# Optimization experiments

Measured on AMD Instinct MI355X. Metric: run time of the kernel, lower is better.

The kernel has to match this reference:

```python
import jax, jax.numpy as jnp
import numpy as np

N = 100000   # nodes
M = N - 1    # tree edges (child -> parent)
EMB = 512    # embedding_size
ENC = 512    # encoder_size


def setup_inputs() -> dict:
    key = jax.random.key(0)
    ks = jax.random.split(key, 10)
    x = jax.random.normal(ks[0], (N, EMB), jnp.float32)
    h = jax.random.normal(ks[1], (N, ENC), jnp.float32)
    c = jax.random.normal(ks[2], (N, ENC), jnp.float32)
    child_idx = jax.random.randint(ks[3], (M,), 0, N)
    parent_idx = jax.random.randint(ks[4], (M,), 0, N)
    s = 0.05
    W_iou = jax.random.normal(ks[5], (3 * ENC, EMB), jnp.float32) * s
    U_iou = jax.random.normal(ks[6], (3 * ENC, ENC), jnp.float32) * s
    b_iou = jnp.zeros((3 * ENC,), jnp.float32)
    U_f_w = jax.random.normal(ks[7], (ENC, ENC), jnp.float32) * s
    U_f_b = jax.random.normal(ks[8], (ENC,), jnp.float32) * s
    return {"x": x, "h": h, "c": c, "child_idx": child_idx,
            "parent_idx": parent_idx, "W_iou": W_iou, "U_iou": U_iou,
            "b_iou": b_iou, "U_f_w": U_f_w, "U_f_b": U_f_b}


def reference(x, h, c, child_idx, parent_idx, W_iou, U_iou, b_iou, U_f_w, U_f_b):
    n = x.shape[0]
    # message_func: gather child states along edges  [M, ENC]
    h_src = h[child_idx]
    c_src = c[child_idx]
    # reduce_func: forget gate per child, ragged sums over children
    f = jax.nn.sigmoid(h_src @ U_f_w.T + U_f_b)               # [M, ENC]
    h_tilde = jax.ops.segment_sum(h_src, parent_idx, num_segments=n)
    c_red = jax.ops.segment_sum(f * c_src, parent_idx, num_segments=n)
    deg = jax.ops.segment_sum(jnp.ones((h_src.shape[0],), x.dtype),
                              parent_idx, num_segments=n)
    has_child = (deg > 0)[:, None]
    # reduce_func overwrites iou with U_iou(h_tilde) for nodes with children;
    # leaves keep the initial W_iou(x).
    iou = jnp.where(has_child, h_tilde @ U_iou.T, x @ W_iou.T) + b_iou
    i, o, u = jnp.split(iou, 3, axis=1)
    c_new = jax.nn.sigmoid(i) * jnp.tanh(u) + jnp.where(has_child, c_red, 0.0)
    h_new = jax.nn.sigmoid(o) * jnp.tanh(c_new)
    return h_new, c_new
```

## Files before the change

kernel.cpp:

```cpp
#include <hip/hip_runtime.h>
#include <stdint.h>

typedef __bf16 bf16x8 __attribute__((ext_vector_type(8)));
typedef float f32x4 __attribute__((ext_vector_type(4)));
typedef unsigned short ushort8 __attribute__((ext_vector_type(8)));

__device__ __forceinline__ float bf2f(unsigned short u) {
  union { uint32_t i; float f; } v; v.i = ((uint32_t)u) << 16; return v.f;
}
__device__ __forceinline__ unsigned short f2bf(float f) {
  union { uint32_t i; float f; } v; v.f = f;
  uint32_t u = v.i;
  return (unsigned short)((u + 0x7fffu + ((u >> 16) & 1u)) >> 16);
}
__device__ __forceinline__ float sigm(float x) { return 1.0f / (1.0f + __expf(-x)); }
__device__ __forceinline__ float tanh_f(float x) { return 1.0f - 2.0f / (__expf(2.0f * x) + 1.0f); }

__device__ __forceinline__ ushort4 cvt4(float4 a) {
  ushort4 o; o.x = f2bf(a.x); o.y = f2bf(a.y); o.z = f2bf(a.z); o.w = f2bf(a.w); return o;
}

__device__ __forceinline__ int xcd_swz(int bid, int nwg) {
  int q = nwg >> 3, r = nwg & 7;
  int x = bid & 7, idx = bid >> 3;
  return (x < r ? x * (q + 1) : r * (q + 1) + (x - r) * q) + idx;
}

__global__ void k_f2bf(const float* __restrict__ src, unsigned short* __restrict__ dst, long long n8) {
  long long t = (long long)blockIdx.x * blockDim.x + threadIdx.x;
  if (t >= n8) return;
  const float4* s = (const float4*)src + t * 2;
  float4 a = s[0], b = s[1];
  ((ushort4*)dst)[t * 2]     = cvt4(a);
  ((ushort4*)dst)[t * 2 + 1] = cvt4(b);
}

__global__ void k_hist(const int* __restrict__ parent, int* __restrict__ deg, int M) {
  int e = blockIdx.x * blockDim.x + threadIdx.x;
  if (e < M) atomicAdd(&deg[parent[e]], 1);
}

__global__ void k_scan1(const int* __restrict__ deg, unsigned long long* __restrict__ ps,
                        unsigned long long* __restrict__ bsum, int Nn) {
  __shared__ unsigned long long tmp[256];
  int t = blockIdx.x * 256 + threadIdx.x;
  int d = (t < Nn) ? deg[t] : 0;
  unsigned long long v = (unsigned long long)(unsigned)d | ((d > 0) ? (1ull << 32) : 0ull);
  tmp[threadIdx.x] = v;
  __syncthreads();
#pragma unroll
  for (int s = 1; s < 256; s <<= 1) {
    unsigned long long a = (threadIdx.x >= (unsigned)s) ? tmp[threadIdx.x - s] : 0;
    __syncthreads();
    tmp[threadIdx.x] += a;
    __syncthreads();
  }
  if (t < Nn) ps[t] = tmp[threadIdx.x] - v;
  if (threadIdx.x == 255) bsum[blockIdx.x] = tmp[255];
}

__global__ void k_scan2(unsigned long long* __restrict__ bsum, int nb,
                        int* __restrict__ meta, int Nn) {
  __shared__ unsigned long long tmp[512];
  int i = threadIdx.x;
  unsigned long long v = (i < nb) ? bsum[i] : 0;
  tmp[i] = v;
  __syncthreads();
#pragma unroll
  for (int s = 1; s < 512; s <<= 1) {
    unsigned long long a = (i >= s) ? tmp[i - s] : 0;
    __syncthreads();
    tmp[i] += a;
    __syncthreads();
  }
  if (i < nb) bsum[i] = tmp[i] - v;
  if (i == 511) {
    int Ni = (int)(tmp[511] >> 32);
    int L0 = ((Ni + 255) >> 8) << 8;
    meta[0] = Ni;
    meta[1] = L0;
    meta[2] = L0 + (Nn - Ni);
  }
}

__global__ void k_scan3(const unsigned long long* __restrict__ ps,
                        const unsigned long long* __restrict__ bsum,
                        const int* __restrict__ meta, const int* __restrict__ deg,
                        int* __restrict__ rs, int* __restrict__ cursor,
                        int* __restrict__ slot, int* __restrict__ nodeof, int Nn) {
  int t = blockIdx.x * 256 + threadIdx.x;
  if (t >= Nn) return;
  unsigned long long p = ps[t] + bsum[blockIdx.x];
  int r  = (int)(p & 0xffffffffull);
  int si = (int)(p >> 32);
  rs[t] = r;
  cursor[t] = r;
  int sl = (deg[t] > 0) ? si : (meta[1] + (t - si));
  slot[t] = sl;
  nodeof[sl] = t;
}

__global__ void k_fill(const int* __restrict__ parent, const int* __restrict__ child,
                       int* __restrict__ cursor, int* __restrict__ childlist, int M) {
  int e = blockIdx.x * blockDim.x + threadIdx.x;
  if (e >= M) return;
  int p = parent[e];
  int pos = atomicAdd(&cursor[p], 1);
  childlist[pos] = child[e];
}

__global__ void k_reduce(const unsigned short* __restrict__ hbuf,
                         const unsigned short* __restrict__ fcb, const float* __restrict__ x,
                         const int* __restrict__ rs, const int* __restrict__ childlist,
                         const int* __restrict__ slot,
                         unsigned short* __restrict__ Zp, unsigned short* __restrict__ credb,
                         int Nn, int M) {
  int p = blockIdx.x * 4 + (threadIdx.x >> 6);
  if (p >= Nn) return;
  int ln = threadIdx.x & 63;
  int j = ln * 8;
  int start = rs[p];
  int end = (p + 1 < Nn) ? rs[p + 1] : M;
  size_t zb = (size_t)slot[p] * 512 + j;
  if (end > start) {
    float hs[8] = {0, 0, 0, 0, 0, 0, 0, 0};
    float cs[8] = {0, 0, 0, 0, 0, 0, 0, 0};
    for (int i = start; i < end; ++i) {
      int ch = childlist[i];
      size_t cb = (size_t)ch * 512 + j;
      ushort8 hv = *(const ushort8*)(hbuf + cb);
      ushort8 fv = *(const ushort8*)(fcb + cb);
#pragma unroll
      for (int q = 0; q < 8; ++q) {
        hs[q] += bf2f(hv[q]);
        cs[q] += bf2f(fv[q]);
      }
    }
    float4 h0 = {hs[0], hs[1], hs[2], hs[3]}, h1 = {hs[4], hs[5], hs[6], hs[7]};
    float4 c0 = {cs[0], cs[1], cs[2], cs[3]}, c1 = {cs[4], cs[5], cs[6], cs[7]};
    ((ushort4*)(Zp + zb))[0] = cvt4(h0);
    ((ushort4*)(Zp + zb))[1] = cvt4(h1);
    size_t cr = (size_t)p * 512 + j;
    ((ushort4*)(credb + cr))[0] = cvt4(c0);
    ((ushort4*)(credb + cr))[1] = cvt4(c1);
  } else {
    const float4* s = (const float4*)(x + (size_t)p * 512 + j);
    float4 x0 = s[0], x1 = s[1];
    ((ushort4*)(Zp + zb))[0] = cvt4(x0);
    ((ushort4*)(Zp + zb))[1] = cvt4(x1);
  }
}

__global__ __launch_bounds__(512)
void k_gemm_f(const unsigned short* __restrict__ A,
              const unsigned short* __restrict__ Bt,
              const float* __restrict__ bias, const float* __restrict__ cmat,
              unsigned short* __restrict__ C, int Mrows) {
  __shared__ __align__(16) unsigned short ldsA[256 * 32];
  __shared__ __align__(16) unsigned short ldsB[128 * 32];
  const int K = 512, ldc = 512;
  const int tid = threadIdx.x;
  const int wv = tid >> 6, ln = tid & 63;
  const int wr = wv >> 1, wc = wv & 1;
  int wg = xcd_swz(blockIdx.x, gridDim.x);
  int rowp = wg >> 2;
  int colp = wg & 3;
  const int row0 = rowp * 256;
  const int col0 = colp * 128;

  f32x4 acc[4][4] = {};

  for (int k0 = 0; k0 < K; k0 += 32) {
#pragma unroll
    for (int rep = 0; rep < 2; ++rep) {
      int cidx = rep * 512 + tid;
      int r  = cidx >> 2;
      int kp = (cidx & 3) * 8;
      int ga = row0 + r; if (ga > Mrows - 1) ga = Mrows - 1;
      const unsigned short* srcA = A + (size_t)ga * K + k0 + kp;
      __builtin_amdgcn_global_load_lds(
          (const __attribute__((address_space(1))) void*)(void*)srcA,
          (__attribute__((address_space(3))) void*)(ldsA + (size_t)cidx * 8),
          16, 0, 0);
    }
    {
      int cidx = tid;
      int r  = cidx >> 2;
      int kp = (cidx & 3) * 8;
      const unsigned short* srcB = Bt + (size_t)(col0 + r) * K + k0 + kp;
      __builtin_amdgcn_global_load_lds(
          (const __attribute__((address_space(1))) void*)(void*)srcB,
          (__attribute__((address_space(3))) void*)(ldsB + (size_t)cidx * 8),
          16, 0, 0);
    }
    __syncthreads();

    bf16x8 af[4], bfr[4];
#pragma unroll
    for (int mi = 0; mi < 4; ++mi)
      af[mi] = *(const bf16x8*)(ldsA + (wr * 64 + mi * 16 + (ln & 15)) * 32 + (ln >> 4) * 8);
#pragma unroll
    for (int ni = 0; ni < 4; ++ni)
      bfr[ni] = *(const bf16x8*)(ldsB + (wc * 64 + ni * 16 + (ln & 15)) * 32 + (ln >> 4) * 8);
#pragma unroll
    for (int mi = 0; mi < 4; ++mi)
#pragma unroll
      for (int ni = 0; ni < 4; ++ni)
        acc[mi][ni] = __builtin_amdgcn_mfma_f32_16x16x32_bf16(bfr[ni], af[mi], acc[mi][ni], 0, 0, 0);
    __syncthreads();
  }

#pragma unroll
  for (int mi = 0; mi < 4; ++mi) {
    int gm = row0 + wr * 64 + mi * 16 + (ln & 15);
    if (gm >= Mrows) continue;
#pragma unroll
    for (int ni = 0; ni < 4; ++ni) {
      int gn = col0 + wc * 64 + ni * 16 + (ln >> 4) * 4;
      float4 bv = *(const float4*)(bias + gn);
      float4 cv = *(const float4*)(cmat + (size_t)gm * ldc + gn);
      ushort4 o;
      o.x = f2bf(sigm(acc[mi][ni][0] + bv.x) * cv.x);
      o.y = f2bf(sigm(acc[mi][ni][1] + bv.y) * cv.y);
      o.z = f2bf(sigm(acc[mi][ni][2] + bv.z) * cv.z);
      o.w = f2bf(sigm(acc[mi][ni][3] + bv.w) * cv.w);
      *(ushort4*)(C + (size_t)gm * ldc + gn) = o;
    }
  }
}

__global__ __launch_bounds__(512)
void k_gemm_iou(const unsigned short* __restrict__ Zp,
                const unsigned short* __restrict__ Ub,
                const unsigned short* __restrict__ Wb,
                const float* __restrict__ bias,
                const int* __restrict__ meta,
                const int* __restrict__ nodeof,
                unsigned short* __restrict__ C) {
  __shared__ __align__(16) unsigned short ldsA[256 * 32];
  __shared__ __align__(16) unsigned short ldsB[128 * 32];
  const int K = 512, ldc = 1536;
  const int tid = threadIdx.x;
  const int wv = tid >> 6, ln = tid & 63;
  const int wr = wv >> 1, wc = wv & 1;
  int wg = xcd_swz(blockIdx.x, gridDim.x);
  int rowp = wg / 12;
  int colp = wg - rowp * 12;
  const int row0 = rowp * 256;
  const int col0 = colp * 128;

  const int Ni = meta[0], L0 = meta[1], lim2 = meta[2];
  const bool internal = row0 < L0;
  const int limit = internal ? Ni : lim2;
  if (row0 >= limit) return;
  const unsigned short* __restrict__ Bt = internal ? Ub : Wb;

  f32x4 acc[4][4] = {};

  for (int k0 = 0; k0 < K; k0 += 32) {
#pragma unroll
    for (int rep = 0; rep < 2; ++rep) {
      int cidx = rep * 512 + tid;
      int r  = cidx >> 2;
      int kp = (cidx & 3) * 8;
      int ga = row0 + r; if (ga > limit - 1) ga = limit - 1;
      const unsigned short* srcA = Zp + (size_t)ga * K + k0 + kp;
      __builtin_amdgcn_global_load_lds(
          (const __attribute__((address_space(1))) void*)(void*)srcA,
          (__attribute__((address_space(3))) void*)(ldsA + (size_t)cidx * 8),
          16, 0, 0);
    }
    {
      int cidx = tid;
      int r  = cidx >> 2;
      int kp = (cidx & 3) * 8;
      const unsigned short* srcB = Bt + (size_t)(col0 + r) * K + k0 + kp;
      __builtin_amdgcn_global_load_lds(
          (const __attribute__((address_space(1))) void*)(void*)srcB,
          (__attribute__((address_space(3))) void*)(ldsB + (size_t)cidx * 8),
          16, 0, 0);
    }
    __syncthreads();

    bf16x8 af[4], bfr[4];
#pragma unroll
    for (int mi = 0; mi < 4; ++mi)
      af[mi] = *(const bf16x8*)(ldsA + (wr * 64 + mi * 16 + (ln & 15)) * 32 + (ln >> 4) * 8);
#pragma unroll
    for (int ni = 0; ni < 4; ++ni)
      bfr[ni] = *(const bf16x8*)(ldsB + (wc * 64 + ni * 16 + (ln & 15)) * 32 + (ln >> 4) * 8);
#pragma unroll
    for (int mi = 0; mi < 4; ++mi)
#pragma unroll
      for (int ni = 0; ni < 4; ++ni)
        acc[mi][ni] = __builtin_amdgcn_mfma_f32_16x16x32_bf16(bfr[ni], af[mi], acc[mi][ni], 0, 0, 0);
    __syncthreads();
  }

#pragma unroll
  for (int mi = 0; mi < 4; ++mi) {
    int m = row0 + wr * 64 + mi * 16 + (ln & 15);
    if (m >= limit) continue;
    int node = nodeof[m];
    size_t ob = (size_t)node * ldc;
#pragma unroll
    for (int ni = 0; ni < 4; ++ni) {
      int gn = col0 + wc * 64 + ni * 16 + (ln >> 4) * 4;
      float4 bv = *(const float4*)(bias + gn);
      ushort4 o;
      o.x = f2bf(acc[mi][ni][0] + bv.x);
      o.y = f2bf(acc[mi][ni][1] + bv.y);
      o.z = f2bf(acc[mi][ni][2] + bv.z);
      o.w = f2bf(acc[mi][ni][3] + bv.w);
      *(ushort4*)(C + ob + gn) = o;
    }
  }
}

__global__ void k_epilogue(const unsigned short* __restrict__ iou,
                           const unsigned short* __restrict__ credb,
                           const int* __restrict__ deg,
                           float* __restrict__ out, int Nn) {
  long long t = (long long)blockIdx.x * blockDim.x + threadIdx.x;
  int n = (int)(t >> 6);
  if (n >= Nn) return;
  int j = ((int)t & 63) * 8;
  size_t ib = (size_t)n * 1536;
  ushort4 iv0 = *(const ushort4*)(iou + ib + j);
  ushort4 iv1 = *(const ushort4*)(iou + ib + j + 4);
  ushort4 ov0 = *(const ushort4*)(iou + ib + 512 + j);
  ushort4 ov1 = *(const ushort4*)(iou + ib + 512 + j + 4);
  ushort4 uv0 = *(const ushort4*)(iou + ib + 1024 + j);
  ushort4 uv1 = *(const ushort4*)(iou + ib + 1024 + j + 4);

  float carr[8] = {0, 0, 0, 0, 0, 0, 0, 0};
  if (deg[n] > 0) {
    size_t cr = (size_t)n * 512 + j;
    ushort4 c0 = *(const ushort4*)(credb + cr);
    ushort4 c1 = *(const ushort4*)(credb + cr + 4);
    carr[0] = bf2f(c0.x); carr[1] = bf2f(c0.y); carr[2] = bf2f(c0.z); carr[3] = bf2f(c0.w);
    carr[4] = bf2f(c1.x); carr[5] = bf2f(c1.y); carr[6] = bf2f(c1.z); carr[7] = bf2f(c1.w);
  }

  float iarr[8] = {bf2f(iv0.x), bf2f(iv0.y), bf2f(iv0.z), bf2f(iv0.w),
                   bf2f(iv1.x), bf2f(iv1.y), bf2f(iv1.z), bf2f(iv1.w)};
  float oarr[8] = {bf2f(ov0.x), bf2f(ov0.y), bf2f(ov0.z), bf2f(ov0.w),
                   bf2f(ov1.x), bf2f(ov1.y), bf2f(ov1.z), bf2f(ov1.w)};
  float uarr[8] = {bf2f(uv0.x), bf2f(uv0.y), bf2f(uv0.z), bf2f(uv0.w),
                   bf2f(uv1.x), bf2f(uv1.y), bf2f(uv1.z), bf2f(uv1.w)};
  float hn[8], cn[8];
#pragma unroll
  for (int q = 0; q < 8; ++q) {
    float cc = sigm(iarr[q]) * tanh_f(uarr[q]) + carr[q];
    cn[q] = cc;
    hn[q] = sigm(oarr[q]) * tanh_f(cc);
  }
  size_t hb = (size_t)n * 512 + j;
  size_t cb = (size_t)Nn * 512 + hb;
  *(float4*)(out + hb)     = make_float4(hn[0], hn[1], hn[2], hn[3]);
  *(float4*)(out + hb + 4) = make_float4(hn[4], hn[5], hn[6], hn[7]);
  *(float4*)(out + cb)     = make_float4(cn[0], cn[1], cn[2], cn[3]);
  *(float4*)(out + cb + 4) = make_float4(cn[4], cn[5], cn[6], cn[7]);
}

extern "C" void kernel_launch(void* const* d_in, const int* in_sizes, int n_in,
                              void* d_out, int out_size, void* d_ws, size_t ws_size,
                              hipStream_t stream) {
  const float* x     = (const float*)d_in[0];
  const float* h     = (const float*)d_in[1];
  const float* c     = (const float*)d_in[2];
  const int* child   = (const int*)d_in[3];
  const int* parent  = (const int*)d_in[4];
  const float* W_iou = (const float*)d_in[5];
  const float* U_iou = (const float*)d_in[6];
  const float* b_iou = (const float*)d_in[7];
  const float* U_f_w = (const float*)d_in[8];
  const float* U_f_b = (const float*)d_in[9];

  const int Nn = in_sizes[0] / 512;
  const int M  = in_sizes[3];

  float* out = (float*)d_out;

  char* ws = (char*)d_ws;
  auto al = [](size_t v) { return (v + 255) & ~(size_t)255; };
  size_t sz0    = al((size_t)Nn * 1536 * 2);
  size_t offZp  = sz0;
  size_t szZp   = al((size_t)(Nn + 256) * 512 * 2);
  size_t offHb  = offZp + szZp;
  size_t szHb   = al((size_t)Nn * 512 * 2);
  size_t offCr  = offHb + szHb;
  size_t szCr   = al((size_t)Nn * 512 * 2);
  size_t offDeg = offCr + szCr;
  size_t szN4   = al((size_t)Nn * 4);
  size_t offRs  = offDeg + szN4;
  size_t offCur = offRs + szN4;
  size_t offSl  = offCur + szN4;
  size_t offNo  = offSl + szN4;
  size_t szNo   = al((size_t)(Nn + 256) * 4);
  size_t offPs  = offNo + szNo;
  size_t szPs   = al((size_t)Nn * 8);
  size_t offCl  = offPs + szPs;
  size_t szCl   = al((size_t)M * 4);
  size_t offBs  = offCl + szCl;
  size_t szBs   = al(512 * 8);
  size_t offMt  = offBs + szBs;
  size_t szMt   = 256;
  size_t offWf  = offMt + szMt;
  size_t szWf   = al(512 * 512 * 2);
  size_t offUb  = offWf + szWf;
  size_t szUw   = al((size_t)1536 * 512 * 2);
  size_t offWb  = offUb + szUw;
  size_t needed = offWb + szUw;
  if (ws_size < needed) return;

  unsigned short* fcb   = (unsigned short*)(ws);
  unsigned short* iou   = (unsigned short*)(ws);
  unsigned short* Zp    = (unsigned short*)(ws + offZp);
  unsigned short* hbuf  = (unsigned short*)(ws + offHb);
  unsigned short* credb = (unsigned short*)(ws + offCr);
  int*            deg   = (int*)(ws + offDeg);
  int*            rs    = (int*)(ws + offRs);
  int*            cursor= (int*)(ws + offCur);
  int*            slot  = (int*)(ws + offSl);
  int*            nodeof= (int*)(ws + offNo);
  unsigned long long* ps   = (unsigned long long*)(ws + offPs);
  int*            clist = (int*)(ws + offCl);
  unsigned long long* bsum = (unsigned long long*)(ws + offBs);
  int*            meta  = (int*)(ws + offMt);
  unsigned short* Wf    = (unsigned short*)(ws + offWf);
  unsigned short* Ub    = (unsigned short*)(ws + offUb);
  unsigned short* Wb    = (unsigned short*)(ws + offWb);

  hipMemsetAsync(deg, 0, (size_t)Nn * 4, stream);

  long long n8h = (long long)Nn * 512 / 8;
  k_f2bf<<<(int)((n8h + 255) / 256), 256, 0, stream>>>(h, hbuf, n8h);
  k_f2bf<<<(512 * 512 / 8 + 255) / 256, 256, 0, stream>>>(U_f_w, Wf, 512 * 512 / 8);
  k_f2bf<<<(1536 * 512 / 8 + 255) / 256, 256, 0, stream>>>(U_iou, Ub, 1536 * 512 / 8);
  k_f2bf<<<(1536 * 512 / 8 + 255) / 256, 256, 0, stream>>>(W_iou, Wb, 1536 * 512 / 8);

  int nb1 = (Nn + 255) / 256;
  k_hist<<<(M + 255) / 256, 256, 0, stream>>>(parent, deg, M);
  k_scan1<<<nb1, 256, 0, stream>>>(deg, ps, bsum, Nn);
  k_scan2<<<1, 512, 0, stream>>>(bsum, nb1, meta, Nn);
  k_scan3<<<nb1, 256, 0, stream>>>(ps, bsum, meta, deg, rs, cursor, slot, nodeof, Nn);
  k_fill<<<(M + 255) / 256, 256, 0, stream>>>(parent, child, cursor, clist, M);

  int nbyF = (Nn + 255) / 256;
  k_gemm_f<<<nbyF * 4, 512, 0, stream>>>(hbuf, Wf, U_f_b, c, fcb, Nn);

  k_reduce<<<(Nn + 3) / 4, 256, 0, stream>>>(hbuf, fcb, x, rs, clist, slot, Zp, credb, Nn, M);

  int nbyI = (Nn >> 8) + 2;
  k_gemm_iou<<<nbyI * 12, 512, 0, stream>>>(Zp, Ub, Wb, b_iou, meta, nodeof, iou);

  k_epilogue<<<(int)(((long long)Nn * 64 + 255) / 256), 256, 0, stream>>>(iou, credb, deg, out, Nn);
}
```

Baseline: 731.6 us.

## Double-buffer LDS tiles in both GEMM kernels to overlap loads with MFMA

Both GEMM kernels now keep two LDS buffers for the A and B tiles. Each iteration issues the global-to-LDS loads for the next K slice before running the MFMAs on the current one, and a single vmcnt wait plus barrier per step replaces the two syncthreads. The goal is to hide global load latency behind matrix compute. In exchange, LDS use per block doubles, which can lower occupancy, and the single barrier relies on the vmcnt wait and the LDS-read ordering being enough to prevent WAR hazards.

```diff
diff --git a/kernel.cpp b/kernel.cpp
--- a/kernel.cpp
+++ b/kernel.cpp
@@ -156,8 +156,8 @@
               const unsigned short* __restrict__ Bt,
               const float* __restrict__ bias, const float* __restrict__ cmat,
               unsigned short* __restrict__ C, int Mrows) {
-  __shared__ __align__(16) unsigned short ldsA[256 * 32];
-  __shared__ __align__(16) unsigned short ldsB[128 * 32];
+  __shared__ __align__(16) unsigned short ldsA[2][256 * 32];
+  __shared__ __align__(16) unsigned short ldsB[2][128 * 32];
   const int K = 512, ldc = 512;
   const int tid = threadIdx.x;
   const int wv = tid >> 6, ln = tid & 63;
@@ -170,7 +170,7 @@
 
   f32x4 acc[4][4] = {};
 
-  for (int k0 = 0; k0 < K; k0 += 32) {
+  auto stage = [&](int buf, int k0) {
 #pragma unroll
     for (int rep = 0; rep < 2; ++rep) {
       int cidx = rep * 512 + tid;
@@ -180,7 +180,7 @@
       const unsigned short* srcA = A + (size_t)ga * K + k0 + kp;
       __builtin_amdgcn_global_load_lds(
           (const __attribute__((address_space(1))) void*)(void*)srcA,
-          (__attribute__((address_space(3))) void*)(ldsA + (size_t)cidx * 8),
+          (__attribute__((address_space(3))) void*)(&ldsA[buf][(size_t)cidx * 8]),
           16, 0, 0);
     }
     {
@@ -190,25 +190,39 @@
       const unsigned short* srcB = Bt + (size_t)(col0 + r) * K + k0 + kp;
       __builtin_amdgcn_global_load_lds(
           (const __attribute__((address_space(1))) void*)(void*)srcB,
-          (__attribute__((address_space(3))) void*)(ldsB + (size_t)cidx * 8),
+          (__attribute__((address_space(3))) void*)(&ldsB[buf][(size_t)cidx * 8]),
           16, 0, 0);
     }
-    __syncthreads();
-
+  };
+
+  auto compute = [&](int buf) {
     bf16x8 af[4], bfr[4];
 #pragma unroll
     for (int mi = 0; mi < 4; ++mi)
-      af[mi] = *(const bf16x8*)(ldsA + (wr * 64 + mi * 16 + (ln & 15)) * 32 + (ln >> 4) * 8);
+      af[mi] = *(const bf16x8*)(&ldsA[buf][(size_t)(wr * 64 + mi * 16 + (ln & 15)) * 32 + (ln >> 4) * 8]);
 #pragma unroll
     for (int ni = 0; ni < 4; ++ni)
-      bfr[ni] = *(const bf16x8*)(ldsB + (wc * 64 + ni * 16 + (ln & 15)) * 32 + (ln >> 4) * 8);
+      bfr[ni] = *(const bf16x8*)(&ldsB[buf][(size_t)(wc * 64 + ni * 16 + (ln & 15)) * 32 + (ln >> 4) * 8]);
 #pragma unroll
     for (int mi = 0; mi < 4; ++mi)
 #pragma unroll
       for (int ni = 0; ni < 4; ++ni)
         acc[mi][ni] = __builtin_amdgcn_mfma_f32_16x16x32_bf16(bfr[ni], af[mi], acc[mi][ni], 0, 0, 0);
-    __syncthreads();
-  }
+  };
+
+  stage(0, 0);
+  asm volatile("s_waitcnt vmcnt(0)" ::: "memory");
+  __builtin_amdgcn_s_barrier();
+  int cur = 0;
+#pragma unroll
+  for (int kt = 0; kt < 15; ++kt) {
+    stage(cur ^ 1, (kt + 1) * 32);
+    compute(cur);
+    asm volatile("s_waitcnt vmcnt(0)" ::: "memory");
+    __builtin_amdgcn_s_barrier();
+    cur ^= 1;
+  }
+  compute(cur);
 
 #pragma unroll
   for (int mi = 0; mi < 4; ++mi) {
@@ -237,8 +251,8 @@
                 const int* __restrict__ meta,
                 const int* __restrict__ nodeof,
                 unsigned short* __restrict__ C) {
-  __shared__ __align__(16) unsigned short ldsA[256 * 32];
-  __shared__ __align__(16) unsigned short ldsB[128 * 32];
+  __shared__ __align__(16) unsigned short ldsA[2][256 * 32];
+  __shared__ __align__(16) unsigned short ldsB[2][128 * 32];
   const int K = 512, ldc = 1536;
   const int tid = threadIdx.x;
   const int wv = tid >> 6, ln = tid & 63;
@@ -257,7 +271,7 @@
 
   f32x4 acc[4][4] = {};
 
-  for (int k0 = 0; k0 < K; k0 += 32) {
+  auto stage = [&](int buf, int k0) {
 #pragma unroll
     for (int rep = 0; rep < 2; ++rep) {
       int cidx = rep * 512 + tid;
@@ -267,7 +281,7 @@
       const unsigned short* srcA = Zp + (size_t)ga * K + k0 + kp;
       __builtin_amdgcn_global_load_lds(
           (const __attribute__((address_space(1))) void*)(void*)srcA,
-          (__attribute__((address_space(3))) void*)(ldsA + (size_t)cidx * 8),
+          (__attribute__((address_space(3))) void*)(&ldsA[buf][(size_t)cidx * 8]),
           16, 0, 0);
     }
     {
@@ -277,25 +291,39 @@
       const unsigned short* srcB = Bt + (size_t)(col0 + r) * K + k0 + kp;
       __builtin_amdgcn_global_load_lds(
           (const __attribute__((address_space(1))) void*)(void*)srcB,
-          (__attribute__((address_space(3))) void*)(ldsB + (size_t)cidx * 8),
+          (__attribute__((address_space(3))) void*)(&ldsB[buf][(size_t)cidx * 8]),
           16, 0, 0);
     }
-    __syncthreads();
-
+  };
+
+  auto compute = [&](int buf) {
     bf16x8 af[4], bfr[4];
 #pragma unroll
     for (int mi = 0; mi < 4; ++mi)
-      af[mi] = *(const bf16x8*)(ldsA + (wr * 64 + mi * 16 + (ln & 15)) * 32 + (ln >> 4) * 8);
+      af[mi] = *(const bf16x8*)(&ldsA[buf][(size_t)(wr * 64 + mi * 16 + (ln & 15)) * 32 + (ln >> 4) * 8]);
 #pragma unroll
     for (int ni = 0; ni < 4; ++ni)
-      bfr[ni] = *(const bf16x8*)(ldsB + (wc * 64 + ni * 16 + (ln & 15)) * 32 + (ln >> 4) * 8);
+      bfr[ni] = *(const bf16x8*)(&ldsB[buf][(size_t)(wc * 64 + ni * 16 + (ln & 15)) * 32 + (ln >> 4) * 8]);
 #pragma unroll
     for (int mi = 0; mi < 4; ++mi)
 #pragma unroll
       for (int ni = 0; ni < 4; ++ni)
         acc[mi][ni] = __builtin_amdgcn_mfma_f32_16x16x32_bf16(bfr[ni], af[mi], acc[mi][ni], 0, 0, 0);
-    __syncthreads();
-  }
+  };
+
+  stage(0, 0);
+  asm volatile("s_waitcnt vmcnt(0)" ::: "memory");
+  __builtin_amdgcn_s_barrier();
+  int cur = 0;
+#pragma unroll
+  for (int kt = 0; kt < 15; ++kt) {
+    stage(cur ^ 1, (kt + 1) * 32);
+    compute(cur);
+    asm volatile("s_waitcnt vmcnt(0)" ::: "memory");
+    __builtin_amdgcn_s_barrier();
+    cur ^= 1;
+  }
+  compute(cur);
 
 #pragma unroll
   for (int mi = 0; mi < 4; ++mi) {
```

After: 724.4 us. No clear change (-1.0%).
